# Kernel optimization log

Measured on AMD Instinct MI355X. Metric: run time of the kernel, lower is better.

Reference implementation:

```python
import jax, jax.numpy as jnp
import numpy as np

N = 65536        # batch (nodes)
IN_SIZE = 256    # irreps1.dim * irreps2.dim = 16*16
OUT_SIZE = 256
NNZ = 2048       # nonzero Clebsch-Gordan entries


def setup_inputs() -> dict:
    key = jax.random.key(0)
    k1, k2, k3, k4 = jax.random.split(key, 4)
    inp = jax.random.normal(k1, (N, IN_SIZE), dtype=jnp.float32)
    scale = jax.random.normal(k2, (NNZ,), dtype=jnp.float32)
    M_in = jax.random.randint(k3, (NNZ,), 0, IN_SIZE, dtype=jnp.int64)
    M = jnp.sort(jax.random.randint(k4, (NNZ,), 0, OUT_SIZE, dtype=jnp.int64))
    return {"input": inp, "scale": scale, "M_in": M_in, "M": M, "out_size": OUT_SIZE}


def reference(input, scale, M_in, M, out_size):
    # sparse_scale: out[n, M[k]] += scale[k] * input[n, M_in[k]]
    gathered = input[:, M_in] * scale  # [N, nnz]
    # segment-sum over the nnz axis into out_size output slots (M is sorted)
    out = jax.ops.segment_sum(gathered.T, M, num_segments=out_size,
                              indices_are_sorted=True).T  # [N, out_size]
    return out
```

## Files before the change

kernel.cpp:

```cpp
#include <hip/hip_runtime.h>

#define IN_SZ   256
#define OUT_SZ  256
#define NNZ_C   2048
#define NB      16

__global__ __launch_bounds__(256, 4)
void sparse_tp_kernel(const float* __restrict__ input,
                      const float* __restrict__ scale,
                      const int*   __restrict__ M_in,
                      const int*   __restrict__ M,
                      float*       __restrict__ out,
                      int N)
{
    __shared__ float s_in[NB * IN_SZ];
    __shared__ float s_scale[NNZ_C];
    __shared__ int   s_min[NNZ_C];
    __shared__ int   s_seg[OUT_SZ + 1];

    const int tid  = threadIdx.x;
    const int base = blockIdx.x * NB;

    {
        const float4* sc4  = reinterpret_cast<const float4*>(scale);
        const int4*   mi4  = reinterpret_cast<const int4*>(M_in);
        float4*       ssc4 = reinterpret_cast<float4*>(s_scale);
        int4*         smi4 = reinterpret_cast<int4*>(s_min);
#pragma unroll
        for (int v = tid; v < NNZ_C / 4; v += 256) {
            ssc4[v] = sc4[v];
            smi4[v] = mi4[v];
        }
    }

    {
        const float4* in4 = reinterpret_cast<const float4*>(input + (size_t)base * IN_SZ);
        float4*       si4 = reinterpret_cast<float4*>(s_in);
#pragma unroll
        for (int v = tid; v < NB * IN_SZ / 4; v += 256) {
            int row = v / (IN_SZ / 4);
            if (base + row < N) si4[v] = in4[v];
        }
    }

    {
        int j  = tid;
        int lo = 0, hi = NNZ_C;
        while (lo < hi) {
            int mid = (lo + hi) >> 1;
            if (M[mid] < j) lo = mid + 1; else hi = mid;
        }
        s_seg[j] = lo;
        if (tid == 0) s_seg[OUT_SZ] = NNZ_C;
    }
    __syncthreads();

    float acc[NB];
#pragma unroll
    for (int i = 0; i < NB; ++i) acc[i] = 0.f;

    const int j  = tid;
    const int k1 = s_seg[j + 1];
    for (int k = s_seg[j]; k < k1; ++k) {
        const float s = s_scale[k];
        const int   m = s_min[k];
#pragma unroll
        for (int i = 0; i < NB; ++i)
            acc[i] += s * s_in[i * IN_SZ + m];
    }

    float* orow = out + (size_t)base * OUT_SZ + j;
#pragma unroll
    for (int i = 0; i < NB; ++i) {
        if (base + i < N) orow[(size_t)i * OUT_SZ] = acc[i];
    }
}

extern "C" void kernel_launch(void* const* d_in, const int* in_sizes, int n_in,
                              void* d_out, int out_size, void* d_ws, size_t ws_size,
                              hipStream_t stream)
{
    const float* input = (const float*)d_in[0];
    const float* scale = (const float*)d_in[1];
    const int*   M_in  = (const int*)d_in[2];
    const int*   M     = (const int*)d_in[3];
    float*       out   = (float*)d_out;

    const int N = in_sizes[0] / IN_SZ;
    const int grid = (N + NB - 1) / NB;

    sparse_tp_kernel<<<grid, 256, 0, stream>>>(input, scale, M_in, M, out, N);
}
```

Baseline: 155.4 us.

## Densify sparse CG weights and compute with bf16 MFMA GEMM

Builds a dense 256x256 weight matrix from the sparse (M, M_in, scale) entries by scatter-add in workspace, converts it to bf16, then runs a tiled bf16 MFMA GEMM with swizzled shared-memory tiles on the input. This replaces the per-thread gather loop over shared memory with matrix-core throughput. It adds three small preprocessing launches and converts fp32 activations and weights to bf16, which loses precision relative to the fp32 reference. Atomic scatter also makes the summation order of duplicate entries nondeterministic.

```diff
diff --git a/kernel.cpp b/kernel.cpp
--- a/kernel.cpp
+++ b/kernel.cpp
@@ -1,9 +1,135 @@
 #include <hip/hip_runtime.h>
+#include <hip/hip_bf16.h>
 
 #define IN_SZ   256
 #define OUT_SZ  256
 #define NNZ_C   2048
 #define NB      16
+
+typedef __attribute__((ext_vector_type(8))) short bf16x8;
+typedef __attribute__((ext_vector_type(4))) float f32x4;
+
+static __device__ __forceinline__ short f2bf(float f) {
+    __hip_bfloat16 h = __float2bfloat16(f);
+    return (short)__builtin_bit_cast(unsigned short, h);
+}
+
+
+__global__ void zero_kernel(float* __restrict__ w) {
+    int i = blockIdx.x * 256 + threadIdx.x;
+    ((float4*)w)[i] = (float4){0.f, 0.f, 0.f, 0.f};
+}
+
+__global__ void scatter_kernel(const float* __restrict__ scale,
+                               const int* __restrict__ M_in,
+                               const int* __restrict__ M,
+                               float* __restrict__ w) {
+    int k = blockIdx.x * 256 + threadIdx.x;
+    if (k < NNZ_C) atomicAdd(&w[M[k] * IN_SZ + M_in[k]], scale[k]);
+}
+
+__global__ void cvt_kernel(const float* __restrict__ w, unsigned short* __restrict__ wb) {
+    int i = blockIdx.x * 256 + threadIdx.x;
+    float4 v = ((const float4*)w)[i];
+    ushort4 o;
+    o.x = (unsigned short)f2bf(v.x);
+    o.y = (unsigned short)f2bf(v.y);
+    o.z = (unsigned short)f2bf(v.z);
+    o.w = (unsigned short)f2bf(v.w);
+    ((ushort4*)wb)[i] = o;
+}
+
+
+#define BM 128
+#define BK 64
+
+__global__ __launch_bounds__(512, 2)
+void gemm_kernel(const float* __restrict__ input,
+                 const unsigned short* __restrict__ wbf,
+                 float* __restrict__ out)
+{
+    __shared__ unsigned short sA[BM * BK];
+    __shared__ unsigned short sB[OUT_SZ * BK];
+
+    const int tid  = threadIdx.x;
+    const int lane = tid & 63;
+    const int wid  = tid >> 6;
+    const int wm   = wid >> 2;
+    const int wn   = wid & 3;
+    const long blockRow = (long)blockIdx.x * BM;
+
+    f32x4 acc[4][4];
+#pragma unroll
+    for (int m = 0; m < 4; ++m)
+#pragma unroll
+        for (int n = 0; n < 4; ++n)
+            acc[m][n] = (f32x4){0.f, 0.f, 0.f, 0.f};
+
+    for (int kt = 0; kt < IN_SZ / BK; ++kt) {
+        __syncthreads();
+#pragma unroll
+        for (int it = 0; it < 2; ++it) {
+            int idx = tid + it * 512;
+            int row = idx >> 3, c8 = idx & 7;
+            const float4* g = (const float4*)(input + (blockRow + row) * IN_SZ + kt * BK + c8 * 8);
+            float4 v0 = g[0], v1 = g[1];
+            bf16x8 u;
+            u[0] = f2bf(v0.x); u[1] = f2bf(v0.y); u[2] = f2bf(v0.z); u[3] = f2bf(v0.w);
+            u[4] = f2bf(v1.x); u[5] = f2bf(v1.y); u[6] = f2bf(v1.z); u[7] = f2bf(v1.w);
+            int lb = (row * 128 + c8 * 16) ^ ((row & 7) << 4);
+            *(bf16x8*)((char*)sA + lb) = u;
+        }
+#pragma unroll
+        for (int it = 0; it < 4; ++it) {
+            int idx = tid + it * 512;
+            int col = idx >> 3, k8 = idx & 7;
+            bf16x8 u = *(const bf16x8*)(wbf + col * IN_SZ + kt * BK + k8 * 8);
+            int lb = (col * 128 + k8 * 16) ^ ((col & 7) << 4);
+            *(bf16x8*)((char*)sB + lb) = u;
+        }
+        __syncthreads();
+
+        bf16x8 af[2][4], bfr[2][4];
+#pragma unroll
+        for (int kf = 0; kf < 2; ++kf) {
+#pragma unroll
+            for (int m = 0; m < 4; ++m) {
+                int row  = wm * 64 + m * 16 + (lane & 15);
+                int koff = kf * 32 + (lane >> 4) * 8;
+                int lb = (row * 128 + koff * 2) ^ ((row & 7) << 4);
+                af[kf][m] = *(const bf16x8*)((const char*)sA + lb);
+            }
+#pragma unroll
+            for (int n = 0; n < 4; ++n) {
+                int col  = wn * 64 + n * 16 + (lane & 15);
+                int koff = kf * 32 + (lane >> 4) * 8;
+                int lb = (col * 128 + koff * 2) ^ ((col & 7) << 4);
+                bfr[kf][n] = *(const bf16x8*)((const char*)sB + lb);
+            }
+        }
+#pragma unroll
+        for (int kf = 0; kf < 2; ++kf)
+#pragma unroll
+            for (int m = 0; m < 4; ++m)
+#pragma unroll
+                for (int n = 0; n < 4; ++n)
+                    acc[m][n] = __builtin_amdgcn_mfma_f32_16x16x32_bf16(
+                        af[kf][m], bfr[kf][n], acc[m][n], 0, 0, 0);
+    }
+
+#pragma unroll
+    for (int m = 0; m < 4; ++m) {
+        int row0 = wm * 64 + m * 16 + ((lane >> 4) << 2);
+#pragma unroll
+        for (int n = 0; n < 4; ++n) {
+            int col = wn * 64 + n * 16 + (lane & 15);
+#pragma unroll
+            for (int r = 0; r < 4; ++r)
+                out[(blockRow + row0 + r) * OUT_SZ + col] = acc[m][n][r];
+        }
+    }
+}
+
 
 __global__ __launch_bounds__(256, 4)
 void sparse_tp_kernel(const float* __restrict__ input,
@@ -26,30 +152,19 @@
         const int4*   mi4  = reinterpret_cast<const int4*>(M_in);
         float4*       ssc4 = reinterpret_cast<float4*>(s_scale);
         int4*         smi4 = reinterpret_cast<int4*>(s_min);
-#pragma unroll
-        for (int v = tid; v < NNZ_C / 4; v += 256) {
-            ssc4[v] = sc4[v];
-            smi4[v] = mi4[v];
-        }
-    }
-
+        for (int v = tid; v < NNZ_C / 4; v += 256) { ssc4[v] = sc4[v]; smi4[v] = mi4[v]; }
+    }
     {
         const float4* in4 = reinterpret_cast<const float4*>(input + (size_t)base * IN_SZ);
         float4*       si4 = reinterpret_cast<float4*>(s_in);
-#pragma unroll
         for (int v = tid; v < NB * IN_SZ / 4; v += 256) {
             int row = v / (IN_SZ / 4);
             if (base + row < N) si4[v] = in4[v];
         }
     }
-
     {
-        int j  = tid;
-        int lo = 0, hi = NNZ_C;
-        while (lo < hi) {
-            int mid = (lo + hi) >> 1;
-            if (M[mid] < j) lo = mid + 1; else hi = mid;
-        }
+        int j = tid, lo = 0, hi = NNZ_C;
+        while (lo < hi) { int mid = (lo + hi) >> 1; if (M[mid] < j) lo = mid + 1; else hi = mid; }
         s_seg[j] = lo;
         if (tid == 0) s_seg[OUT_SZ] = NNZ_C;
     }
@@ -59,22 +174,21 @@
 #pragma unroll
     for (int i = 0; i < NB; ++i) acc[i] = 0.f;
 
-    const int j  = tid;
+    const int j = tid;
     const int k1 = s_seg[j + 1];
     for (int k = s_seg[j]; k < k1; ++k) {
         const float s = s_scale[k];
         const int   m = s_min[k];
 #pragma unroll
-        for (int i = 0; i < NB; ++i)
-            acc[i] += s * s_in[i * IN_SZ + m];
+        for (int i = 0; i < NB; ++i) acc[i] += s * s_in[i * IN_SZ + m];
     }
 
     float* orow = out + (size_t)base * OUT_SZ + j;
 #pragma unroll
-    for (int i = 0; i < NB; ++i) {
+    for (int i = 0; i < NB; ++i)
         if (base + i < N) orow[(size_t)i * OUT_SZ] = acc[i];
-    }
-}
+}
+
 
 extern "C" void kernel_launch(void* const* d_in, const int* in_sizes, int n_in,
                               void* d_out, int out_size, void* d_ws, size_t ws_size,
@@ -87,7 +201,15 @@
     float*       out   = (float*)d_out;
 
     const int N = in_sizes[0] / IN_SZ;
-    const int grid = (N + NB - 1) / NB;
-
-    sparse_tp_kernel<<<grid, 256, 0, stream>>>(input, scale, M_in, M, out, N);
-}
+
+    if (ws_size >= (size_t)(384 * 1024) && (N % BM) == 0) {
+        float*          wf = (float*)d_ws;
+        unsigned short* wb = (unsigned short*)((char*)d_ws + 256 * 1024);
+        zero_kernel   <<<64,     256, 0, stream>>>(wf);
+        scatter_kernel<<<8,      256, 0, stream>>>(scale, M_in, M, wf);
+        cvt_kernel    <<<64,     256, 0, stream>>>(wf, wb);
+        gemm_kernel   <<<N / BM, 512, 0, stream>>>(input, wb, out);
+    } else {
+        sparse_tp_kernel<<<(N + NB - 1) / NB, 256, 0, stream>>>(input, scale, M_in, M, out, N);
+    }
+}
```

Result: faster. 130.5 us (-16.0%).

## Densify sparse weights and compute via bf16 MFMA GEMM

Applied to the files above, without the earlier changes.

Adds a prep kernel that scatters the sparse scale entries into a dense 256x256 weight matrix, stored in bf16 in MFMA fragment order in workspace. A second kernel then computes the output as a dense GEMM with 16x16x32 bf16 MFMA, converting input rows to bf16 on load. This replaces the LDS-bound gather/accumulate loop with matrix-core work. It reduces precision to bf16 and depends on workspace size and N being divisible by 64, falling back to the old kernel otherwise.

```diff
diff --git a/kernel.cpp b/kernel.cpp
--- a/kernel.cpp
+++ b/kernel.cpp
@@ -1,9 +1,108 @@
 #include <hip/hip_runtime.h>
+#include <hip/hip_bf16.h>
 
 #define IN_SZ   256
 #define OUT_SZ  256
 #define NNZ_C   2048
 #define NB      16
+#define BMG     64
+
+typedef __attribute__((ext_vector_type(8))) short bf16x8;
+typedef __attribute__((ext_vector_type(4))) float f32x4;
+
+static __device__ __forceinline__ short f2bf(float f) {
+    __hip_bfloat16 h = __float2bfloat16(f);
+    return (short)__builtin_bit_cast(unsigned short, h);
+}
+
+
+__global__ void build_w(const float* __restrict__ scale,
+                        const int*   __restrict__ M_in,
+                        const int*   __restrict__ M,
+                        unsigned short* __restrict__ wb)
+{
+    __shared__ float row[IN_SZ];
+    const int j = blockIdx.x;
+    const int t = threadIdx.x;
+
+#pragma unroll
+    for (int i = t; i < IN_SZ; i += 64) row[i] = 0.f;
+    __syncthreads();
+
+#pragma unroll
+    for (int k = t; k < NNZ_C; k += 64)
+        if (M[k] == j) atomicAdd(&row[M_in[k]], scale[k]);
+    __syncthreads();
+
+    const int wn = j >> 6, n = (j >> 4) & 3, l15 = j & 15;
+#pragma unroll
+    for (int kk = t; kk < IN_SZ; kk += 64) {
+        int kt = kk >> 6, kf = (kk >> 5) & 1, lhi = (kk >> 3) & 3, e = kk & 7;
+        int lane = lhi * 16 + l15;
+        int c = (((wn * 4 + n) * 4 + kt) * 2 + kf) * 64 + lane;
+        wb[c * 8 + e] = (unsigned short)f2bf(row[kk]);
+    }
+}
+
+
+__global__ __launch_bounds__(256, 3)
+void gemm_direct(const float* __restrict__ input,
+                 const bf16x8* __restrict__ wfrag,
+                 float* __restrict__ out)
+{
+    const int tid  = threadIdx.x;
+    const int lane = tid & 63;
+    const int wn   = tid >> 6;
+    const int l15  = lane & 15, lhi = lane >> 4;
+    const long row0 = (long)blockIdx.x * BMG;
+
+    f32x4 acc[4][4];
+#pragma unroll
+    for (int m = 0; m < 4; ++m)
+#pragma unroll
+        for (int n = 0; n < 4; ++n)
+            acc[m][n] = (f32x4){0.f, 0.f, 0.f, 0.f};
+
+#pragma unroll
+    for (int kt = 0; kt < 4; ++kt) {
+#pragma unroll
+        for (int kf = 0; kf < 2; ++kf) {
+            bf16x8 afr[4], bfr[4];
+#pragma unroll
+            for (int m = 0; m < 4; ++m) {
+                const float4* p = (const float4*)(input
+                    + (row0 + m * 16 + l15) * IN_SZ + kt * 64 + kf * 32 + lhi * 8);
+                float4 x = p[0], y = p[1];
+                bf16x8 u;
+                u[0] = f2bf(x.x); u[1] = f2bf(x.y); u[2] = f2bf(x.z); u[3] = f2bf(x.w);
+                u[4] = f2bf(y.x); u[5] = f2bf(y.y); u[6] = f2bf(y.z); u[7] = f2bf(y.w);
+                afr[m] = u;
+            }
+#pragma unroll
+            for (int n = 0; n < 4; ++n)
+                bfr[n] = wfrag[(((wn * 4 + n) * 4 + kt) * 2 + kf) * 64 + lane];
+#pragma unroll
+            for (int m = 0; m < 4; ++m)
+#pragma unroll
+                for (int n = 0; n < 4; ++n)
+                    acc[m][n] = __builtin_amdgcn_mfma_f32_16x16x32_bf16(
+                        afr[m], bfr[n], acc[m][n], 0, 0, 0);
+        }
+    }
+
+#pragma unroll
+    for (int m = 0; m < 4; ++m) {
+        long r0 = row0 + m * 16 + lhi * 4;
+#pragma unroll
+        for (int n = 0; n < 4; ++n) {
+            int col = wn * 64 + n * 16 + l15;
+#pragma unroll
+            for (int r = 0; r < 4; ++r)
+                out[(r0 + r) * OUT_SZ + col] = acc[m][n][r];
+        }
+    }
+}
+
 
 __global__ __launch_bounds__(256, 4)
 void sparse_tp_kernel(const float* __restrict__ input,
@@ -26,30 +125,19 @@
         const int4*   mi4  = reinterpret_cast<const int4*>(M_in);
         float4*       ssc4 = reinterpret_cast<float4*>(s_scale);
         int4*         smi4 = reinterpret_cast<int4*>(s_min);
-#pragma unroll
-        for (int v = tid; v < NNZ_C / 4; v += 256) {
-            ssc4[v] = sc4[v];
-            smi4[v] = mi4[v];
-        }
+        for (int v = tid; v < NNZ_C / 4; v += 256) { ssc4[v] = sc4[v]; smi4[v] = mi4[v]; }
     }
-
     {
         const float4* in4 = reinterpret_cast<const float4*>(input + (size_t)base * IN_SZ);
         float4*       si4 = reinterpret_cast<float4*>(s_in);
-#pragma unroll
         for (int v = tid; v < NB * IN_SZ / 4; v += 256) {
             int row = v / (IN_SZ / 4);
             if (base + row < N) si4[v] = in4[v];
         }
     }
-
     {
-        int j  = tid;
-        int lo = 0, hi = NNZ_C;
-        while (lo < hi) {
-            int mid = (lo + hi) >> 1;
-            if (M[mid] < j) lo = mid + 1; else hi = mid;
-        }
+        int j = tid, lo = 0, hi = NNZ_C;
+        while (lo < hi) { int mid = (lo + hi) >> 1; if (M[mid] < j) lo = mid + 1; else hi = mid; }
         s_seg[j] = lo;
         if (tid == 0) s_seg[OUT_SZ] = NNZ_C;
     }
@@ -59,22 +147,21 @@
 #pragma unroll
     for (int i = 0; i < NB; ++i) acc[i] = 0.f;
 
-    const int j  = tid;
+    const int j = tid;
     const int k1 = s_seg[j + 1];
     for (int k = s_seg[j]; k < k1; ++k) {
         const float s = s_scale[k];
         const int   m = s_min[k];
 #pragma unroll
-        for (int i = 0; i < NB; ++i)
-            acc[i] += s * s_in[i * IN_SZ + m];
+        for (int i = 0; i < NB; ++i) acc[i] += s * s_in[i * IN_SZ + m];
     }
 
     float* orow = out + (size_t)base * OUT_SZ + j;
 #pragma unroll
-    for (int i = 0; i < NB; ++i) {
+    for (int i = 0; i < NB; ++i)
         if (base + i < N) orow[(size_t)i * OUT_SZ] = acc[i];
-    }
 }
+
 
 extern "C" void kernel_launch(void* const* d_in, const int* in_sizes, int n_in,
                               void* d_out, int out_size, void* d_ws, size_t ws_size,
@@ -87,7 +174,12 @@
     float*       out   = (float*)d_out;
 
     const int N = in_sizes[0] / IN_SZ;
-    const int grid = (N + NB - 1) / NB;
 
-    sparse_tp_kernel<<<grid, 256, 0, stream>>>(input, scale, M_in, M, out, N);
+    if (ws_size >= (size_t)(128 * 1024) && (N % BMG) == 0) {
+        unsigned short* wb = (unsigned short*)d_ws;
+        build_w    <<<OUT_SZ, 64, 0, stream>>>(scale, M_in, M, wb);
+        gemm_direct<<<N / BMG, 256, 0, stream>>>(input, (const bf16x8*)wb, out);
+    } else {
+        sparse_tp_kernel<<<(N + NB - 1) / NB, 256, 0, stream>>>(input, scale, M_in, M, out, N);
+    }
 }
```

After: 157.9 us. Within noise of the previous version (+1.6%).
